# Optimization experiments

Measured on AMD Instinct MI355X. Metric: run time of the kernel, lower is better.

Reference implementation:

```python
import jax, jax.numpy as jnp
import numpy as np

B, T, V, H = 1, 1024, 32000, 2048
NH, NKV, HD = 8, 4, 256
QS, KVS = NH * HD, NKV * HD
I, L = 8192, 2
SCALE = 256.0 ** -0.5          # query_pre_attn_scalar ** -0.5
ATTN_CAP, FINAL_CAP = 50.0, 30.0
WIN, EPS, THETA = 512, 1e-6, 10000.0
NEG = -2.3819763e38


def setup_inputs() -> dict:
    key = jax.random.key(0)
    ks = jax.random.split(key, 12)
    s = 0.02
    return {
        "tokens": jax.random.randint(ks[0], (B, T), 0, V, dtype=jnp.int32),
        "embed": jax.random.normal(ks[1], (V, H), jnp.float32) * s,
        "qkv_w": jax.random.normal(ks[2], (L, (NH + 2 * NKV) * HD, H), jnp.float32) * s,
        "o_w": jax.random.normal(ks[3], (L, H, NH * HD), jnp.float32) * s,
        "gate_w": jax.random.normal(ks[4], (L, I, H), jnp.float32) * s,
        "up_w": jax.random.normal(ks[5], (L, I, H), jnp.float32) * s,
        "down_w": jax.random.normal(ks[6], (L, H, I), jnp.float32) * s,
        "ln_in": jax.random.normal(ks[7], (L, H), jnp.float32) * s,   # RMSNorm weight (zeros-init offset)
        "ln_pa": jax.random.normal(ks[8], (L, H), jnp.float32) * s,
        "ln_pre": jax.random.normal(ks[9], (L, H), jnp.float32) * s,
        "ln_post": jax.random.normal(ks[10], (L, H), jnp.float32) * s,
        "ln_f": jax.random.normal(ks[11], (H,), jnp.float32) * s,
    }


def rmsnorm(x, w):
    x = x.astype(jnp.float32)
    n = x * jax.lax.rsqrt(jnp.mean(x * x, axis=-1, keepdims=True) + EPS)
    return n * (1.0 + w)  # add_unit_offset=True


def rope(x, cos, sin):
    # x: [B, T, N, HD]; split-half complex rotary as in apply_rotary_emb
    x1, x2 = jnp.split(x, 2, axis=-1)
    c = cos[None, :, None, :]
    s = sin[None, :, None, :]
    return jnp.concatenate([x1 * c - x2 * s, x1 * s + x2 * c], axis=-1)


def reference(tokens, embed, qkv_w, o_w, gate_w, up_w, down_w,
              ln_in, ln_pa, ln_pre, ln_post, ln_f):
    pos = jnp.arange(T)
    inv = 1.0 / (THETA ** (jnp.arange(0, HD, 2, dtype=jnp.float32) / HD))  # [HD/2]
    ang = pos.astype(jnp.float32)[:, None] * inv[None, :]
    cos, sin = jnp.cos(ang), jnp.sin(ang)

    i, j = pos[:, None], pos[None, :]
    causal = j <= i
    mask_global = jnp.where(causal, 0.0, NEG).astype(jnp.float32)
    mask_local = jnp.where(causal & (i - j < WIN), 0.0, NEG).astype(jnp.float32)
    masks = [mask_local, mask_global]  # layer 0: LOCAL_SLIDING, layer 1: GLOBAL

    x = embed[tokens] * jnp.sqrt(jnp.float32(H))  # Gemma embedding normalizer

    for l in range(L):
        h = rmsnorm(x, ln_in[l])
        qkv = jnp.einsum('bth,oh->bto', h, qkv_w[l])
        q = qkv[..., :QS].reshape(B, T, NH, HD)
        k = qkv[..., QS:QS + KVS].reshape(B, T, NKV, HD)
        v = qkv[..., QS + KVS:].reshape(B, T, NKV, HD)
        q = rope(q, cos, sin)
        k = rope(k, cos, sin)
        # prefill: kv_write_indices=arange(T) -> cache == current k/v
        k = jnp.repeat(k, NH // NKV, axis=2)  # GQA repeat_interleave over heads
        v = jnp.repeat(v, NH // NKV, axis=2)
        scores = jnp.einsum('bqhd,bkhd->bhqk', q * SCALE, k)
        scores = jnp.tanh(scores / ATTN_CAP) * ATTN_CAP
        scores = scores + masks[l][None, None]
        attn = jax.nn.softmax(scores.astype(jnp.float32), axis=-1)
        out = jnp.einsum('bhqk,bkhd->bqhd', attn, v).reshape(B, T, NH * HD)
        out = jnp.einsum('bto,ho->bth', out, o_w[l])
        x = x + rmsnorm(out, ln_pa[l])

        h = rmsnorm(x, ln_pre[l])
        gate = jax.nn.gelu(jnp.einsum('bth,ih->bti', h, gate_w[l]), approximate=True)
        up = jnp.einsum('bth,ih->bti', h, up_w[l])
        ff = jnp.einsum('bti,hi->bth', gate * up, down_w[l])
        x = x + rmsnorm(ff, ln_post[l])

    x = rmsnorm(x, ln_f)
    logits = jnp.einsum('bth,vh->btv', x, embed)
    logits = jnp.tanh(logits / FINAL_CAP) * FINAL_CAP  # final_logit_softcapping
    return logits
```

## Files before the change

kernel.cpp:

```cpp
#include <hip/hip_runtime.h>
#include <hip/hip_bf16.h>
#include <math.h>

typedef unsigned short u16;
typedef __attribute__((ext_vector_type(8))) short bf16x8;
typedef __attribute__((ext_vector_type(4))) float f32x4;
typedef __attribute__((ext_vector_type(4))) u16 u16x4;
typedef __attribute__((ext_vector_type(4))) unsigned u32x4;

#define T_SEQ 1024
#define HDIM  2048
#define NHEAD 8
#define NKVH  4
#define HSZ   256
#define ISZ   8192
#define NVOC  32000

#define GLDS(src, dst) __builtin_amdgcn_global_load_lds( \
    (const __attribute__((address_space(1))) void*)(src), \
    (__attribute__((address_space(3))) void*)(dst), 16, 0, 0)

__device__ __forceinline__ u16 f2bf(float f) {
    union { float f; unsigned u; } v; v.f = f;
    return (u16)((v.u + 0x7fffu + ((v.u >> 16) & 1u)) >> 16);
}
__device__ __forceinline__ float bf2f(u16 h) {
    union { unsigned u; float f; } v; v.u = (unsigned)h << 16; return v.f;
}

__device__ __forceinline__ unsigned cvt_pk_bf16(float a, float b) {
    unsigned r;
    asm("v_cvt_pk_bf16_f32 %0, %1, %2" : "=v"(r) : "v"(a), "v"(b));
    return r;
}

__device__ __forceinline__ float fast_tanh(float x) {
    float e = __expf(-2.0f * fabsf(x));
    float t = (1.0f - e) / (1.0f + e);
    return copysignf(t, x);
}

__device__ __forceinline__ f32x4 mfma16(bf16x8 a, bf16x8 b, f32x4 c) {
    return __builtin_amdgcn_mfma_f32_16x16x32_bf16(a, b, c, 0, 0, 0);
}

template<int EPI, typename CT>
__global__ __launch_bounds__(512, 1)
void gemm_f(const u16* __restrict__ A, int lda,
            const float* __restrict__ B, int ldb,
            CT* __restrict__ C, int ldc, long sC, int K,
            const float* __restrict__ UP)
{
    extern __shared__ char lds[];
    const int t = threadIdx.x;
    const int lane = t & 63, wid = t >> 6;
    const int z = blockIdx.z;
    A += (long)z * K;
    B += (long)z * K;
    C += (long)z * sC;

    const int nwg = gridDim.x * gridDim.y;
    int flat = blockIdx.y * gridDim.x + blockIdx.x;
    {
        const int q = nwg >> 3, r = nwg & 7;
        const int xcd = flat & 7, loc = flat >> 3;
        flat = (xcd < r ? xcd * (q + 1) : r * (q + 1) + (xcd - r) * q) + loc;
    }
    const int gm = gridDim.y;
    const long m0 = (long)(flat % gm) * 256;
    const long n0 = (long)(flat / gm) * 128;

    const int ar = t >> 3;
    const int asl = ((t & 7) ^ (ar & 7)) * 8;
    const u16* gA0 = A + (m0 + ar)       * (long)lda + asl;
    const u16* gA1 = A + (m0 + 64 + ar)  * (long)lda + asl;
    const u16* gA2 = A + (m0 + 128 + ar) * (long)lda + asl;
    const u16* gA3 = A + (m0 + 192 + ar) * (long)lda + asl;
    const int br = t >> 4;
    const int bsl = ((t & 15) ^ (br & 15)) * 4;
    const float* gB0 = B + (n0 + br)      * (long)ldb + bsl;
    const float* gB1 = B + (n0 + 32 + br) * (long)ldb + bsl;
    const float* gB2 = B + (n0 + 64 + br) * (long)ldb + bsl;
    const float* gB3 = B + (n0 + 96 + br) * (long)ldb + bsl;

    auto stage = [&](int kt) {
        const long ko = (long)kt * 64;
        char* d = lds + (kt & 1) * 65536 + t * 16;
        GLDS(gA0 + ko, d);
        GLDS(gA1 + ko, d + 8192);
        GLDS(gA2 + ko, d + 16384);
        GLDS(gA3 + ko, d + 24576);
        GLDS(gB0 + ko, d + 32768);
        GLDS(gB1 + ko, d + 40960);
        GLDS(gB2 + ko, d + 49152);
        GLDS(gB3 + ko, d + 57344);
    };

    f32x4 acc[4][4] = {};
    const int fr = lane & 15, kq = lane >> 4;
    const int wm = wid >> 1, wn = wid & 1;
    const int ps0 = ((kq)     ^ (fr & 7)) * 8;
    const int ps1 = ((4 + kq) ^ (fr & 7)) * 8;

    const int KT = K >> 6;
    stage(0);
    stage(1);

    for (int kt = 0; kt < KT; ++kt) {
        if (kt < KT - 1) asm volatile("s_waitcnt vmcnt(8)" ::: "memory");
        else             asm volatile("s_waitcnt vmcnt(0)" ::: "memory");
        __builtin_amdgcn_s_barrier();

        const u16*   As = (const u16*)(lds + (kt & 1) * 65536);
        const float* Bs = (const float*)(lds + (kt & 1) * 65536 + 32768);
        const int arow = wm * 64 + fr;
        const int brow = wn * 64 + fr;

        #pragma unroll
        for (int kk = 0; kk < 2; ++kk) {
            const int ps = kk ? ps1 : ps0;
            const int G = 8 * kk + 2 * kq;
            const int sa = G ^ fr, sb = (G + 1) ^ fr;
            bf16x8 af[4], bfv[4];
            #pragma unroll
            for (int mi = 0; mi < 4; ++mi)
                af[mi] = *(const bf16x8*)(As + (arow + mi * 16) * 64 + ps);
            #pragma unroll
            for (int ni = 0; ni < 4; ++ni) {
                const float* rp = Bs + (brow + ni * 16) * 64;
                f32x4 v0 = *(const f32x4*)(rp + sa * 4);
                f32x4 v1 = *(const f32x4*)(rp + sb * 4);
                u32x4 bw;
                bw.x = cvt_pk_bf16(v0.x, v0.y);
                bw.y = cvt_pk_bf16(v0.z, v0.w);
                bw.z = cvt_pk_bf16(v1.x, v1.y);
                bw.w = cvt_pk_bf16(v1.z, v1.w);
                bfv[ni] = __builtin_bit_cast(bf16x8, bw);
            }
            __builtin_amdgcn_s_setprio(1);
            #pragma unroll
            for (int mi = 0; mi < 4; ++mi)
                #pragma unroll
                for (int ni = 0; ni < 4; ++ni)
                    acc[mi][ni] = mfma16(af[mi], bfv[ni], acc[mi][ni]);
            __builtin_amdgcn_s_setprio(0);
        }
        __builtin_amdgcn_s_barrier();
        if (kt + 2 < KT) stage(kt + 2);
    }

    const int crb = kq * 4, ccol = fr;
    #pragma unroll
    for (int mi = 0; mi < 4; ++mi) {
        #pragma unroll
        for (int rr = 0; rr < 4; ++rr) {
            const long row = m0 + wm * 64 + mi * 16 + crb + rr;
            CT* cp = C + row * ldc + n0 + wn * 64 + ccol;
            #pragma unroll
            for (int ni = 0; ni < 4; ++ni) {
                float v = acc[mi][ni][rr];
                if constexpr (EPI == 1) {
                    cp[ni * 16] = (CT)(fast_tanh(v * (1.0f / 30.0f)) * 30.0f);
                } else if constexpr (EPI == 2) {
                    const float* upp = UP + row * (long)ldc + n0 + wn * 64 + ccol;
                    const float tt = fast_tanh(0.79788456f * (v + 0.044715f * v * v * v));
                    const float g = 0.5f * v * (1.0f + tt);
                    ((u16*)cp)[ni * 16] = f2bf(g * upp[ni * 16]);
                } else {
                    cp[ni * 16] = (CT)v;
                }
            }
        }
    }
}

template<int EPI, typename CT>
__global__ __launch_bounds__(256)
void gemm_bt(const u16* __restrict__ A, int lda, long sA,
             const u16* __restrict__ B, int ldb, long sB, int bshift,
             CT* __restrict__ C, int ldc, long sC, int K,
             int swin, int tflag)
{
    __shared__ u16 As[128 * 32];
    __shared__ u16 Bs[128 * 32];
    const int tid = threadIdx.x;
    const int lane = tid & 63, wid = tid >> 6;
    const int z = blockIdx.z;
    A += (long)z * sA;
    B += (long)(z >> bshift) * sB;
    C += (long)z * sC;

    const int nwg = gridDim.x * gridDim.y;
    int flat = blockIdx.y * gridDim.x + blockIdx.x;
    {
        const int q = nwg >> 3, r = nwg & 7;
        const int xcd = flat & 7, loc = flat >> 3;
        flat = (xcd < r ? xcd * (q + 1) : r * (q + 1) + (xcd - r) * q) + loc;
    }
    const int gm = gridDim.y;
    const long m0 = (long)(flat % gm) * 128;
    const long n0 = (long)(flat / gm) * 128;

    if (swin > 0) {
        if (n0 > m0 + 127) return;
        if (m0 - (n0 + 127) >= swin) return;
    }
    int klo = 0, khi = K;
    if (tflag > 0) {
        const long hi = m0 + 128;
        if (hi < khi) khi = (int)hi;
        const long lo = m0 - (long)tflag + 1;
        klo = lo > 0 ? (int)(lo & ~31L) : 0;
    }

    f32x4 acc[4][4] = {};

    const int ar = tid >> 2, ac = (tid & 3) * 8;
    const u16* gA0 = A + (m0 + ar) * lda + ac;
    const u16* gB0 = B + (n0 + ar) * (long)ldb + ac;
    const long a64 = 64L * lda, b64 = 64L * ldb;

    const int fr = lane & 15, fk = (lane >> 4) * 8;
    const int wm = (wid >> 1) * 64, wn = (wid & 1) * 64;

    for (int k0 = klo; k0 < khi; k0 += 32) {
        GLDS(gA0 + k0,       &As[tid * 8]);
        GLDS(gA0 + a64 + k0, &As[2048 + tid * 8]);
        GLDS(gB0 + k0,       &Bs[tid * 8]);
        GLDS(gB0 + b64 + k0, &Bs[2048 + tid * 8]);
        __syncthreads();
        bf16x8 af[4], bfv[4];
        #pragma unroll
        for (int mi = 0; mi < 4; ++mi)
            af[mi] = *(const bf16x8*)(&As[(wm + mi * 16 + fr) * 32 + fk]);
        #pragma unroll
        for (int ni = 0; ni < 4; ++ni)
            bfv[ni] = *(const bf16x8*)(&Bs[(wn + ni * 16 + fr) * 32 + fk]);
        #pragma unroll
        for (int mi = 0; mi < 4; ++mi)
            #pragma unroll
            for (int ni = 0; ni < 4; ++ni)
                acc[mi][ni] = mfma16(af[mi], bfv[ni], acc[mi][ni]);
        __syncthreads();
    }

    const int crb = (lane >> 4) * 4, ccol = lane & 15;
    #pragma unroll
    for (int mi = 0; mi < 4; ++mi) {
        #pragma unroll
        for (int rr = 0; rr < 4; ++rr) {
            const long row = m0 + wm + mi * 16 + crb + rr;
            CT* cp = C + row * ldc + n0 + wn + ccol;
            #pragma unroll
            for (int ni = 0; ni < 4; ++ni) {
                float v = acc[mi][ni][rr];
                if (EPI == 1) v = fast_tanh(v * (1.0f / 30.0f)) * 30.0f;
                if constexpr (sizeof(CT) == 2) cp[ni * 16] = f2bf(v);
                else                           cp[ni * 16] = v;
            }
        }
    }
}

__global__ __launch_bounds__(256)
void embed_scale(const int* __restrict__ tok, const float* __restrict__ emb,
                 float* __restrict__ x)
{
    const int t = blockIdx.x, tid = threadIdx.x;
    const long src = (long)tok[t] * HDIM;
    f32x4 a = *(const f32x4*)(emb + src + tid * 8);
    f32x4 b = *(const f32x4*)(emb + src + tid * 8 + 4);
    a *= 45.254834f; b *= 45.254834f;
    *(f32x4*)(x + (long)t * HDIM + tid * 8) = a;
    *(f32x4*)(x + (long)t * HDIM + tid * 8 + 4) = b;
}

__device__ __forceinline__ float block_sum(float v, float* red) {
    #pragma unroll
    for (int o = 32; o; o >>= 1) v += __shfl_xor(v, o);
    const int tid = threadIdx.x;
    if ((tid & 63) == 0) red[tid >> 6] = v;
    __syncthreads();
    return red[0] + red[1] + red[2] + red[3];
}

__global__ __launch_bounds__(256)
void rmsnorm_bf16(const float* __restrict__ x, const float* __restrict__ w,
                  u16* __restrict__ out)
{
    __shared__ float red[4];
    const int t = blockIdx.x, tid = threadIdx.x;
    const float* row = x + (long)t * HDIM;
    f32x4 a = *(const f32x4*)(row + tid * 8);
    f32x4 b = *(const f32x4*)(row + tid * 8 + 4);
    float ss = a.x*a.x + a.y*a.y + a.z*a.z + a.w*a.w
             + b.x*b.x + b.y*b.y + b.z*b.z + b.w*b.w;
    ss = block_sum(ss, red);
    const float r = rsqrtf(ss * (1.0f / HDIM) + 1e-6f);
    f32x4 wa = *(const f32x4*)(w + tid * 8);
    f32x4 wb = *(const f32x4*)(w + tid * 8 + 4);
    u16x4 o0, o1;
    o0.x = f2bf(a.x * r * (1.0f + wa.x)); o0.y = f2bf(a.y * r * (1.0f + wa.y));
    o0.z = f2bf(a.z * r * (1.0f + wa.z)); o0.w = f2bf(a.w * r * (1.0f + wa.w));
    o1.x = f2bf(b.x * r * (1.0f + wb.x)); o1.y = f2bf(b.y * r * (1.0f + wb.y));
    o1.z = f2bf(b.z * r * (1.0f + wb.z)); o1.w = f2bf(b.w * r * (1.0f + wb.w));
    *(u16x4*)(out + (long)t * HDIM + tid * 8) = o0;
    *(u16x4*)(out + (long)t * HDIM + tid * 8 + 4) = o1;
}

__global__ __launch_bounds__(256)
void add_rms_rms(float* __restrict__ x, const float* __restrict__ y,
                 const float* __restrict__ w1, const float* __restrict__ w2,
                 u16* __restrict__ out, int nsplit, long stride)
{
    __shared__ float red[4];
    const int t = blockIdx.x, tid = threadIdx.x;
    const float* yr = y + (long)t * HDIM;
    f32x4 a = *(const f32x4*)(yr + tid * 8);
    f32x4 b = *(const f32x4*)(yr + tid * 8 + 4);
    for (int s = 1; s < nsplit; ++s) {
        a += *(const f32x4*)(yr + s * stride + tid * 8);
        b += *(const f32x4*)(yr + s * stride + tid * 8 + 4);
    }
    float ss = a.x*a.x + a.y*a.y + a.z*a.z + a.w*a.w
             + b.x*b.x + b.y*b.y + b.z*b.z + b.w*b.w;
    ss = block_sum(ss, red);
    const float r1 = rsqrtf(ss * (1.0f / HDIM) + 1e-6f);
    f32x4 wa = *(const f32x4*)(w1 + tid * 8);
    f32x4 wb = *(const f32x4*)(w1 + tid * 8 + 4);
    float* xr = x + (long)t * HDIM;
    f32x4 xa = *(const f32x4*)(xr + tid * 8);
    f32x4 xb = *(const f32x4*)(xr + tid * 8 + 4);
    xa.x += a.x * r1 * (1.0f + wa.x); xa.y += a.y * r1 * (1.0f + wa.y);
    xa.z += a.z * r1 * (1.0f + wa.z); xa.w += a.w * r1 * (1.0f + wa.w);
    xb.x += b.x * r1 * (1.0f + wb.x); xb.y += b.y * r1 * (1.0f + wb.y);
    xb.z += b.z * r1 * (1.0f + wb.z); xb.w += b.w * r1 * (1.0f + wb.w);
    *(f32x4*)(xr + tid * 8) = xa;
    *(f32x4*)(xr + tid * 8 + 4) = xb;
    __syncthreads();
    float ss2 = xa.x*xa.x + xa.y*xa.y + xa.z*xa.z + xa.w*xa.w
              + xb.x*xb.x + xb.y*xb.y + xb.z*xb.z + xb.w*xb.w;
    ss2 = block_sum(ss2, red);
    const float r2 = rsqrtf(ss2 * (1.0f / HDIM) + 1e-6f);
    f32x4 va = *(const f32x4*)(w2 + tid * 8);
    f32x4 vb = *(const f32x4*)(w2 + tid * 8 + 4);
    u16x4 o0, o1;
    o0.x = f2bf(xa.x * r2 * (1.0f + va.x)); o0.y = f2bf(xa.y * r2 * (1.0f + va.y));
    o0.z = f2bf(xa.z * r2 * (1.0f + va.z)); o0.w = f2bf(xa.w * r2 * (1.0f + va.w));
    o1.x = f2bf(xb.x * r2 * (1.0f + vb.x)); o1.y = f2bf(xb.y * r2 * (1.0f + vb.y));
    o1.z = f2bf(xb.z * r2 * (1.0f + vb.z)); o1.w = f2bf(xb.w * r2 * (1.0f + vb.w));
    *(u16x4*)(out + (long)t * HDIM + tid * 8) = o0;
    *(u16x4*)(out + (long)t * HDIM + tid * 8 + 4) = o1;
}

#define QKV_STRIDE (1024L * 4096)

__global__ __launch_bounds__(256)
void qkv_post(const float* __restrict__ qkv, u16* __restrict__ qb,
              u16* __restrict__ kb)
{
    const int t = blockIdx.x, tid = threadIdx.x;
    const float* row = qkv + (long)t * 4096;
    const float ft = (float)t;
    #pragma unroll
    for (int it = 0; it < 4; ++it) {
        const int p = tid + it * 256;
        const int nh = p >> 7, d = p & 127;
        const float inv = powf(10000.0f, -(float)d * (1.0f / 128.0f));
        const float ang = ft * inv;
        const float c = cosf(ang), s = sinf(ang);
        const int i1 = nh * 256 + d, i2 = i1 + 128;
        const float x1 = row[i1] + row[i1 + QKV_STRIDE];
        const float x2 = row[i2] + row[i2 + QKV_STRIDE];
        const long ob = ((long)nh * T_SEQ + t) * HSZ;
        qb[ob + d]       = f2bf((x1 * c - x2 * s) * 0.0625f);
        qb[ob + 128 + d] = f2bf((x1 * s + x2 * c) * 0.0625f);
    }
    #pragma unroll
    for (int it = 0; it < 2; ++it) {
        const int p = tid + it * 256;
        const int kv = p >> 7, d = p & 127;
        const float inv = powf(10000.0f, -(float)d * (1.0f / 128.0f));
        const float ang = ft * inv;
        const float c = cosf(ang), s = sinf(ang);
        const int i1 = 2048 + kv * 256 + d, i2 = i1 + 128;
        const float x1 = row[i1] + row[i1 + QKV_STRIDE];
        const float x2 = row[i2] + row[i2 + QKV_STRIDE];
        const long ob = ((long)kv * T_SEQ + t) * HSZ;
        kb[ob + d]       = f2bf(x1 * c - x2 * s);
        kb[ob + 128 + d] = f2bf(x1 * s + x2 * c);
    }
}

__global__ __launch_bounds__(256)
void v_transpose(const float* __restrict__ qkvb, u16* __restrict__ vT)
{
    __shared__ u16 tile[64][65];
    const int t0 = blockIdx.x * 64, d0 = blockIdx.y * 64, kv = blockIdx.z;
    const int lane = threadIdx.x & 63, w = threadIdx.x >> 6;
    #pragma unroll
    for (int i = 0; i < 16; ++i) {
        const int t = w * 16 + i;
        const long idx = (long)(t0 + t) * 4096 + 3072 + kv * 256 + d0 + lane;
        tile[t][lane] = f2bf(qkvb[idx] + qkvb[idx + QKV_STRIDE]);
    }
    __syncthreads();
    #pragma unroll
    for (int i = 0; i < 16; ++i) {
        const int d = w * 16 + i;
        vT[((long)kv * HSZ + d0 + d) * T_SEQ + t0 + lane] = tile[lane][d];
    }
}

__global__ __launch_bounds__(256)
void softmax_mask(const float* __restrict__ sc, u16* __restrict__ pr, int win)
{
    __shared__ float redm[4], reds[4];
    const int i = blockIdx.x, h = blockIdx.y, tid = threadIdx.x;
    const long base = ((long)h * T_SEQ + i) * T_SEQ;
    f32x4 sv = *(const f32x4*)(sc + base + tid * 4);
    float vals[4];
    #pragma unroll
    for (int j = 0; j < 4; ++j) {
        const int col = tid * 4 + j;
        const float s = fast_tanh(sv[j] * 0.02f) * 50.0f;
        const bool valid = (col <= i) && ((i - col) < win);
        vals[j] = valid ? s : -3.0e38f;
    }
    float m = fmaxf(fmaxf(vals[0], vals[1]), fmaxf(vals[2], vals[3]));
    #pragma unroll
    for (int o = 32; o; o >>= 1) m = fmaxf(m, __shfl_xor(m, o));
    if ((tid & 63) == 0) redm[tid >> 6] = m;
    __syncthreads();
    m = fmaxf(fmaxf(redm[0], redm[1]), fmaxf(redm[2], redm[3]));
    float sum = 0.0f;
    #pragma unroll
    for (int j = 0; j < 4; ++j) { vals[j] = __expf(vals[j] - m); sum += vals[j]; }
    #pragma unroll
    for (int o = 32; o; o >>= 1) sum += __shfl_xor(sum, o);
    if ((tid & 63) == 0) reds[tid >> 6] = sum;
    __syncthreads();
    sum = reds[0] + reds[1] + reds[2] + reds[3];
    const float inv = 1.0f / sum;
    u16x4 o4;
    #pragma unroll
    for (int j = 0; j < 4; ++j) o4[j] = f2bf(vals[j] * inv);
    *(u16x4*)(pr + base + tid * 4) = o4;
}

extern "C" void kernel_launch(void* const* d_in, const int* in_sizes, int n_in,
                              void* d_out, int out_size, void* d_ws, size_t ws_size,
                              hipStream_t stream)
{
    (void)in_sizes; (void)n_in; (void)out_size; (void)ws_size;
    const int*   tokens = (const int*)  d_in[0];
    const float* emb    = (const float*)d_in[1];
    const float* qkv_w  = (const float*)d_in[2];
    const float* o_w    = (const float*)d_in[3];
    const float* gate_w = (const float*)d_in[4];
    const float* up_w   = (const float*)d_in[5];
    const float* down_w = (const float*)d_in[6];
    const float* ln_in  = (const float*)d_in[7];
    const float* ln_pa  = (const float*)d_in[8];
    const float* ln_pre = (const float*)d_in[9];
    const float* ln_post= (const float*)d_in[10];
    const float* ln_f   = (const float*)d_in[11];
    float* logits = (float*)d_out;

    char* base = (char*)d_ws;
    size_t off = 0;
    auto alloc = [&](size_t b) { char* p = base + off; off += (b + 255) & ~(size_t)255; return p; };

    float* x    = (float*)alloc((size_t)T_SEQ * HDIM * 4);
    u16*   hb   = (u16*)  alloc((size_t)T_SEQ * HDIM * 2);
    u16*   qb   = (u16*)  alloc((size_t)NHEAD * T_SEQ * HSZ * 2);
    u16*   kb   = (u16*)  alloc((size_t)NKVH * T_SEQ * HSZ * 2);
    u16*   vT   = (u16*)  alloc((size_t)NKVH * HSZ * T_SEQ * 2);
    u16*   ao   = (u16*)  alloc((size_t)T_SEQ * HDIM * 2);
    u16*   pb   = (u16*)  alloc((size_t)T_SEQ * ISZ * 2);
    char*  big  = alloc((size_t)2 * T_SEQ * ISZ * 4);
    float* P    = (float*)big;
    float* sc   = (float*)big;
    u16*   pr   = (u16*)(big + (size_t)NHEAD * T_SEQ * T_SEQ * 4);
    float* ub   = (float*)(big + (size_t)T_SEQ * ISZ * 4);

    const size_t LDSF = 2 * 65536;
    const long s2048 = 1024L * 2048;
    const int BIGWIN = 1 << 29;

    embed_scale<<<T_SEQ, 256, 0, stream>>>(tokens, emb, x);
    for (int l = 0; l < 2; ++l) {
        const int win = (l == 0) ? 512 : BIGWIN;
        if (l == 0)
            rmsnorm_bf16<<<T_SEQ, 256, 0, stream>>>(x, ln_in, hb);
        gemm_f<0, float><<<dim3(32, 4, 2), 512, LDSF, stream>>>(
            hb, HDIM, qkv_w + (size_t)l * 4096 * HDIM, HDIM, P, 4096, QKV_STRIDE, 1024, ub);
        qkv_post<<<T_SEQ, 256, 0, stream>>>(P, qb, kb);
        v_transpose<<<dim3(16, 4, 4), 256, 0, stream>>>(P, vT);
        gemm_bt<0, float><<<dim3(8, 8, NHEAD), 256, 0, stream>>>(
            qb, HSZ, (long)T_SEQ * HSZ, kb, HSZ, (long)T_SEQ * HSZ, 1,
            sc, T_SEQ, (long)T_SEQ * T_SEQ, HSZ, win, 0);
        softmax_mask<<<dim3(T_SEQ, NHEAD, 1), 256, 0, stream>>>(
            sc, pr, l == 0 ? 512 : (1 << 30));
        gemm_bt<0, u16><<<dim3(2, 8, NHEAD), 256, 0, stream>>>(
            pr, T_SEQ, (long)T_SEQ * T_SEQ, vT, T_SEQ, (long)HSZ * T_SEQ, 1,
            ao, HDIM, (long)HSZ, T_SEQ, 0, win);
        gemm_f<0, float><<<dim3(16, 4, 4), 512, LDSF, stream>>>(
            ao, HDIM, o_w + (size_t)l * HDIM * HDIM, HDIM, P, HDIM, s2048, 512, ub);
        add_rms_rms<<<T_SEQ, 256, 0, stream>>>(
            x, P, ln_pa + l * HDIM, ln_pre + l * HDIM, hb, 4, s2048);
        gemm_f<0, float><<<dim3(64, 4, 1), 512, LDSF, stream>>>(
            hb, HDIM, up_w + (size_t)l * ISZ * HDIM, HDIM, ub, ISZ, 0, HDIM, ub);
        gemm_f<2, u16><<<dim3(64, 4, 1), 512, LDSF, stream>>>(
            hb, HDIM, gate_w + (size_t)l * ISZ * HDIM, HDIM, pb, ISZ, 0, HDIM, ub);
        gemm_f<0, float><<<dim3(16, 4, 4), 512, LDSF, stream>>>(
            pb, ISZ, down_w + (size_t)l * HDIM * ISZ, ISZ, P, HDIM, s2048, 2048, ub);
        const float* w2 = (l == 0) ? (ln_in + HDIM) : ln_f;
        add_rms_rms<<<T_SEQ, 256, 0, stream>>>(
            x, P, ln_post + l * HDIM, w2, hb, 4, s2048);
    }
    gemm_f<1, float><<<dim3(250, 4, 1), 512, LDSF, stream>>>(
        hb, HDIM, emb, HDIM, logits, NVOC, 0, HDIM, ub);
}
```

Baseline: 784.0 us.

## Widen weight GEMM tile to 256x256 with K=32 triple-buffered LDS pipeline

```diff
diff --git a/kernel.cpp b/kernel.cpp
--- a/kernel.cpp
+++ b/kernel.cpp
@@ -46,7 +46,7 @@
 
 template<int EPI, typename CT>
 __global__ __launch_bounds__(512, 1)
-void gemm_f(const u16* __restrict__ A, int lda,
+void gemm_w(const u16* __restrict__ A, int lda,
             const float* __restrict__ B, int ldb,
             CT* __restrict__ C, int ldc, long sC, int K,
             const float* __restrict__ UP)
@@ -68,97 +68,92 @@
     }
     const int gm = gridDim.y;
     const long m0 = (long)(flat % gm) * 256;
-    const long n0 = (long)(flat / gm) * 128;
-
-    const int ar = t >> 3;
-    const int asl = ((t & 7) ^ (ar & 7)) * 8;
+    const long n0 = (long)(flat / gm) * 256;
+
+    const int ar = t >> 2;
+    const int ak = (ar ^ (ar >> 2)) & 3;
+    const int asl = ((t & 3) ^ ak) * 8;
     const u16* gA0 = A + (m0 + ar)       * (long)lda + asl;
-    const u16* gA1 = A + (m0 + 64 + ar)  * (long)lda + asl;
-    const u16* gA2 = A + (m0 + 128 + ar) * (long)lda + asl;
-    const u16* gA3 = A + (m0 + 192 + ar) * (long)lda + asl;
-    const int br = t >> 4;
-    const int bsl = ((t & 15) ^ (br & 15)) * 4;
-    const float* gB0 = B + (n0 + br)      * (long)ldb + bsl;
-    const float* gB1 = B + (n0 + 32 + br) * (long)ldb + bsl;
-    const float* gB2 = B + (n0 + 64 + br) * (long)ldb + bsl;
-    const float* gB3 = B + (n0 + 96 + br) * (long)ldb + bsl;
+    const u16* gA1 = A + (m0 + 128 + ar) * (long)lda + asl;
+    const int brr = t >> 3;
+    const int bk = (brr ^ (brr >> 3)) & 7;
+    const int bsl = ((t & 7) ^ bk) * 4;
+    const float* gB0 = B + (n0 + brr)       * (long)ldb + bsl;
+    const float* gB1 = B + (n0 + 64 + brr)  * (long)ldb + bsl;
+    const float* gB2 = B + (n0 + 128 + brr) * (long)ldb + bsl;
+    const float* gB3 = B + (n0 + 192 + brr) * (long)ldb + bsl;
 
     auto stage = [&](int kt) {
-        const long ko = (long)kt * 64;
-        char* d = lds + (kt & 1) * 65536 + t * 16;
+        const long ko = (long)kt * 32;
+        char* d = lds + (kt % 3) * 49152 + t * 16;
         GLDS(gA0 + ko, d);
         GLDS(gA1 + ko, d + 8192);
-        GLDS(gA2 + ko, d + 16384);
-        GLDS(gA3 + ko, d + 24576);
-        GLDS(gB0 + ko, d + 32768);
-        GLDS(gB1 + ko, d + 40960);
-        GLDS(gB2 + ko, d + 49152);
-        GLDS(gB3 + ko, d + 57344);
+        GLDS(gB0 + ko, d + 16384);
+        GLDS(gB1 + ko, d + 24576);
+        GLDS(gB2 + ko, d + 32768);
+        GLDS(gB3 + ko, d + 40960);
     };
 
-    f32x4 acc[4][4] = {};
+    f32x4 acc[8][4] = {};
     const int fr = lane & 15, kq = lane >> 4;
-    const int wm = wid >> 1, wn = wid & 1;
-    const int ps0 = ((kq)     ^ (fr & 7)) * 8;
-    const int ps1 = ((4 + kq) ^ (fr & 7)) * 8;
-
-    const int KT = K >> 6;
+    const int wm = wid >> 2, wn = wid & 3;
+    const int KT = K >> 5;
+
     stage(0);
-    stage(1);
+    if (KT > 1) stage(1);
+    if (KT > 2) stage(2);
 
     for (int kt = 0; kt < KT; ++kt) {
-        if (kt < KT - 1) asm volatile("s_waitcnt vmcnt(8)" ::: "memory");
-        else             asm volatile("s_waitcnt vmcnt(0)" ::: "memory");
+        if (kt < KT - 2)       asm volatile("s_waitcnt vmcnt(12)" ::: "memory");
+        else if (kt == KT - 2) asm volatile("s_waitcnt vmcnt(6)" ::: "memory");
+        else                   asm volatile("s_waitcnt vmcnt(0)" ::: "memory");
         __builtin_amdgcn_s_barrier();
 
-        const u16*   As = (const u16*)(lds + (kt & 1) * 65536);
-        const float* Bs = (const float*)(lds + (kt & 1) * 65536 + 32768);
-        const int arow = wm * 64 + fr;
-        const int brow = wn * 64 + fr;
-
-        #pragma unroll
-        for (int kk = 0; kk < 2; ++kk) {
-            const int ps = kk ? ps1 : ps0;
-            const int G = 8 * kk + 2 * kq;
-            const int sa = G ^ fr, sb = (G + 1) ^ fr;
-            bf16x8 af[4], bfv[4];
+        const u16*   As = (const u16*)(lds + (kt % 3) * 49152);
+        const float* Bs = (const float*)(lds + (kt % 3) * 49152 + 16384);
+
+        bf16x8 af[8], bfv[4];
+        #pragma unroll
+        for (int mi = 0; mi < 8; ++mi) {
+            const int rA = wm * 128 + mi * 16 + fr;
+            const int sA = kq ^ ((rA ^ (rA >> 2)) & 3);
+            af[mi] = *(const bf16x8*)(As + rA * 32 + sA * 8);
+        }
+        #pragma unroll
+        for (int ni = 0; ni < 4; ++ni) {
+            const int rB = wn * 64 + ni * 16 + fr;
+            const int kB = (rB ^ (rB >> 3)) & 7;
+            const float* rp = Bs + rB * 32;
+            f32x4 v0 = *(const f32x4*)(rp + ((2 * kq)     ^ kB) * 4);
+            f32x4 v1 = *(const f32x4*)(rp + ((2 * kq + 1) ^ kB) * 4);
+            u32x4 bw;
+            bw.x = cvt_pk_bf16(v0.x, v0.y);
+            bw.y = cvt_pk_bf16(v0.z, v0.w);
+            bw.z = cvt_pk_bf16(v1.x, v1.y);
+            bw.w = cvt_pk_bf16(v1.z, v1.w);
+            bfv[ni] = __builtin_bit_cast(bf16x8, bw);
+        }
+        __builtin_amdgcn_s_setprio(1);
+        #pragma unroll
+        for (int mi = 0; mi < 8; ++mi)
             #pragma unroll
-            for (int mi = 0; mi < 4; ++mi)
-                af[mi] = *(const bf16x8*)(As + (arow + mi * 16) * 64 + ps);
-            #pragma unroll
-            for (int ni = 0; ni < 4; ++ni) {
-                const float* rp = Bs + (brow + ni * 16) * 64;
-                f32x4 v0 = *(const f32x4*)(rp + sa * 4);
-                f32x4 v1 = *(const f32x4*)(rp + sb * 4);
-                u32x4 bw;
-                bw.x = cvt_pk_bf16(v0.x, v0.y);
-                bw.y = cvt_pk_bf16(v0.z, v0.w);
-                bw.z = cvt_pk_bf16(v1.x, v1.y);
-                bw.w = cvt_pk_bf16(v1.z, v1.w);
-                bfv[ni] = __builtin_bit_cast(bf16x8, bw);
-            }
-            __builtin_amdgcn_s_setprio(1);
-            #pragma unroll
-            for (int mi = 0; mi < 4; ++mi)
-                #pragma unroll
-                for (int ni = 0; ni < 4; ++ni)
-                    acc[mi][ni] = mfma16(af[mi], bfv[ni], acc[mi][ni]);
-            __builtin_amdgcn_s_setprio(0);
-        }
+            for (int ni = 0; ni < 4; ++ni)
+                acc[mi][ni] = mfma16(af[mi], bfv[ni], acc[mi][ni]);
+        __builtin_amdgcn_s_setprio(0);
         __builtin_amdgcn_s_barrier();
-        if (kt + 2 < KT) stage(kt + 2);
+        if (kt + 3 < KT) stage(kt + 3);
     }
 
     const int crb = kq * 4, ccol = fr;
     #pragma unroll
-    for (int mi = 0; mi < 4; ++mi) {
+    for (int mj = 0; mj < 8; ++mj) {
         #pragma unroll
         for (int rr = 0; rr < 4; ++rr) {
-            const long row = m0 + wm * 64 + mi * 16 + crb + rr;
+            const long row = m0 + wm * 128 + mj * 16 + crb + rr;
             CT* cp = C + row * ldc + n0 + wn * 64 + ccol;
             #pragma unroll
             for (int ni = 0; ni < 4; ++ni) {
-                float v = acc[mi][ni][rr];
+                float v = acc[mj][ni][rr];
                 if constexpr (EPI == 1) {
                     cp[ni * 16] = (CT)(fast_tanh(v * (1.0f / 30.0f)) * 30.0f);
                 } else if constexpr (EPI == 2) {
@@ -484,7 +479,7 @@
     u16*   pr   = (u16*)(big + (size_t)NHEAD * T_SEQ * T_SEQ * 4);
     float* ub   = (float*)(big + (size_t)T_SEQ * ISZ * 4);
 
-    const size_t LDSF = 2 * 65536;
+    const size_t LDSW = 3 * 49152;
     const long s2048 = 1024L * 2048;
     const int BIGWIN = 1 << 29;
 
@@ -493,7 +488,7 @@
         const int win = (l == 0) ? 512 : BIGWIN;
         if (l == 0)
             rmsnorm_bf16<<<T_SEQ, 256, 0, stream>>>(x, ln_in, hb);
-        gemm_f<0, float><<<dim3(32, 4, 2), 512, LDSF, stream>>>(
+        gemm_w<0, float><<<dim3(16, 4, 2), 512, LDSW, stream>>>(
             hb, HDIM, qkv_w + (size_t)l * 4096 * HDIM, HDIM, P, 4096, QKV_STRIDE, 1024, ub);
         qkv_post<<<T_SEQ, 256, 0, stream>>>(P, qb, kb);
         v_transpose<<<dim3(16, 4, 4), 256, 0, stream>>>(P, vT);
@@ -505,20 +500,20 @@
         gemm_bt<0, u16><<<dim3(2, 8, NHEAD), 256, 0, stream>>>(
             pr, T_SEQ, (long)T_SEQ * T_SEQ, vT, T_SEQ, (long)HSZ * T_SEQ, 1,
             ao, HDIM, (long)HSZ, T_SEQ, 0, win);
-        gemm_f<0, float><<<dim3(16, 4, 4), 512, LDSF, stream>>>(
+        gemm_w<0, float><<<dim3(8, 4, 4), 512, LDSW, stream>>>(
             ao, HDIM, o_w + (size_t)l * HDIM * HDIM, HDIM, P, HDIM, s2048, 512, ub);
         add_rms_rms<<<T_SEQ, 256, 0, stream>>>(
             x, P, ln_pa + l * HDIM, ln_pre + l * HDIM, hb, 4, s2048);
-        gemm_f<0, float><<<dim3(64, 4, 1), 512, LDSF, stream>>>(
+        gemm_w<0, float><<<dim3(32, 4, 1), 512, LDSW, stream>>>(
             hb, HDIM, up_w + (size_t)l * ISZ * HDIM, HDIM, ub, ISZ, 0, HDIM, ub);
-        gemm_f<2, u16><<<dim3(64, 4, 1), 512, LDSF, stream>>>(
+        gemm_w<2, u16><<<dim3(32, 4, 1), 512, LDSW, stream>>>(
             hb, HDIM, gate_w + (size_t)l * ISZ * HDIM, HDIM, pb, ISZ, 0, HDIM, ub);
-        gemm_f<0, float><<<dim3(16, 4, 4), 512, LDSF, stream>>>(
+        gemm_w<0, float><<<dim3(8, 4, 4), 512, LDSW, stream>>>(
             pb, ISZ, down_w + (size_t)l * HDIM * ISZ, ISZ, P, HDIM, s2048, 2048, ub);
         const float* w2 = (l == 0) ? (ln_in + HDIM) : ln_f;
         add_rms_rms<<<T_SEQ, 256, 0, stream>>>(
             x, P, ln_post + l * HDIM, w2, hb, 4, s2048);
     }
-    gemm_f<1, float><<<dim3(250, 4, 1), 512, LDSF, stream>>>(
+    gemm_w<1, float><<<dim3(125, 4, 1), 512, LDSW, stream>>>(
         hb, HDIM, emb, HDIM, logits, NVOC, 0, HDIM, ub);
 }
```

Result: slower. 1.088 ms (+38.7%).
